# Kernel tuning notes

Measured on AMD Instinct MI355X. Metric: run time of the kernel, lower is better.

## Reference

```python
import jax, jax.numpy as jnp
import numpy as np

HEAD = 8
D_Q = 64
NEG_INF = -1e9
EPS = 1e-9


def setup_inputs() -> dict:
    key = jax.random.key(0)
    ks = jax.random.split(key, 5)
    bs, seq_len, d_model = 4, 1024, 512
    context = jax.random.normal(ks[0], (bs, seq_len, d_model), dtype=jnp.float32)
    attention_mask = jnp.ones((bs, seq_len), dtype=jnp.int32)
    # nn.Linear default init: U(-1/sqrt(fan_in), 1/sqrt(fan_in))
    bound = 1.0 / np.sqrt(d_model)
    Wq = jax.random.uniform(ks[1], (HEAD * D_Q, d_model), jnp.float32, -bound, bound)
    bq = jax.random.uniform(ks[2], (HEAD * D_Q,), jnp.float32, -bound, bound)
    Wk = jax.random.uniform(ks[3], (HEAD * D_Q, d_model), jnp.float32, -bound, bound)
    bk = jax.random.uniform(ks[4], (HEAD * D_Q,), jnp.float32, -bound, bound)
    return {"context": context, "attention_mask": attention_mask,
            "Wq": Wq, "bq": bq, "Wk": Wk, "bk": bk}


def reference(context, attention_mask, Wq, bq, Wk, bk):
    bs, seq_len, d_model = context.shape
    # structural masks
    after_mask = jnp.eye(seq_len, k=1, dtype=jnp.int32)    # superdiagonal
    prev_mask = jnp.eye(seq_len, k=-1, dtype=jnp.int32)    # subdiagonal
    self_mask = jnp.eye(seq_len, dtype=jnp.int32)          # diagonal
    summing_op = jnp.triu(jnp.ones((seq_len, seq_len), jnp.float32))  # upper-tri ones

    # attention_mask & (after + prev): (bs,1,1,S) & (S,S) -> (bs,1,S,S)
    mask = attention_mask[:, None, None, :] & (after_mask + prev_mask)

    # projections -> (bs, head, seq, d_q)
    q = (context @ Wq.T + bq).reshape(bs, seq_len, HEAD, D_Q).transpose(0, 2, 1, 3)
    k = (context @ Wk.T + bk).reshape(bs, seq_len, HEAD, D_Q).transpose(0, 2, 1, 3)

    scores = jnp.einsum('bhqd,bhkd->bhqk', q, k) / d_model
    scores = jnp.where(mask == 0, NEG_INF, scores)
    scores = jax.nn.softmax(scores, axis=-1)

    # geometric-mean fusion of forward/backward neighbor scores
    phrasal_attn = jnp.sqrt(scores * jnp.swapaxes(scores, -2, -1) + EPS)
    # prior_attn = 0 (default): phrasal_attn = 0 + (1-0)*phrasal_attn

    # log-cumsum via triangular matmuls
    p = jnp.where(after_mask == 0, 0.0, jnp.log(phrasal_attn + EPS))  # (bs,h,S,S)
    p = jnp.einsum('bhij,jk->bhik', p, summing_op)
    attn = jnp.exp(jnp.einsum('ij,bhjk->bhik', summing_op, p))
    # zero out on-and-below diagonal (keep strict upper triangle)
    strict_upper = summing_op.astype(jnp.int32) - self_mask
    attn = jnp.where(strict_upper == 0, 0.0, attn)
    attn = attn + jnp.swapaxes(attn, -2, -1) + jnp.where(self_mask == 0, EPS, phrasal_attn)
    return (attn, phrasal_attn)
```

## Files before the change

kernel.cpp:

```cpp
#include <hip/hip_runtime.h>
#include <hip/hip_bf16.h>

#define BS 4
#define SEQ 1024
#define DM 512
#define NQK 1024
#define NROW (BS*SEQ)
#define EPS 1e-9f
#define SQRTEPS 3.16227766e-5f

typedef __attribute__((ext_vector_type(8))) short short8;
typedef __attribute__((ext_vector_type(4))) float floatx4;

__global__ __launch_bounds__(256) void convert_kernel(
    const float* __restrict__ ctx, const float* __restrict__ Wq,
    const float* __restrict__ Wk, unsigned short* __restrict__ Xbf,
    unsigned short* __restrict__ Wbf)
{
    int idx = blockIdx.x * 256 + threadIdx.x;
    {
        unsigned int u = __float_as_uint(ctx[idx]);
        Xbf[idx] = (unsigned short)((u + 0x7fffu + ((u >> 16) & 1u)) >> 16);
    }
    if (idx < DM * DM) {
        unsigned int a = __float_as_uint(Wq[idx]);
        Wbf[idx] = (unsigned short)((a + 0x7fffu + ((a >> 16) & 1u)) >> 16);
        unsigned int c = __float_as_uint(Wk[idx]);
        Wbf[DM * DM + idx] = (unsigned short)((c + 0x7fffu + ((c >> 16) & 1u)) >> 16);
    }
}

#define BM 64
#define BN 64
#define BK 32
#define LDA 40

__global__ __launch_bounds__(256) void gemm_qk(
    const unsigned short* __restrict__ X, const unsigned short* __restrict__ W,
    const float* __restrict__ bq, const float* __restrict__ bk,
    float* __restrict__ QK)
{
    __shared__ unsigned short As[BM * LDA];
    __shared__ unsigned short Bs[BN * LDA];

    const int tid  = threadIdx.x;
    const int bm   = blockIdx.x;
    const int bn   = blockIdx.y;
    const int wave = tid >> 6;
    const int lane = tid & 63;
    const int wm   = wave >> 1, wn = wave & 1;
    const int lr   = lane & 15;
    const int kg   = lane >> 4;

    const int srow = tid >> 2;
    const int skc  = (tid & 3) << 3;
    const unsigned short* Xp = X + (size_t)(bm * BM + srow) * DM + skc;
    const unsigned short* Wp = W + (size_t)(bn * BN + srow) * DM + skc;

    floatx4 acc[2][2] = {};

    for (int k0 = 0; k0 < DM; k0 += BK) {
        uint4 va = *(const uint4*)(Xp + k0);
        uint4 vb = *(const uint4*)(Wp + k0);
        __syncthreads();
        *(uint4*)(As + srow * LDA + skc) = va;
        *(uint4*)(Bs + srow * LDA + skc) = vb;
        __syncthreads();

        short8 a[2], b[2];
        #pragma unroll
        for (int mi = 0; mi < 2; ++mi)
            a[mi] = *(const short8*)(As + (wm * 32 + mi * 16 + lr) * LDA + kg * 8);
        #pragma unroll
        for (int ni = 0; ni < 2; ++ni)
            b[ni] = *(const short8*)(Bs + (wn * 32 + ni * 16 + lr) * LDA + kg * 8);
        #pragma unroll
        for (int mi = 0; mi < 2; ++mi)
            #pragma unroll
            for (int ni = 0; ni < 2; ++ni)
                acc[mi][ni] = __builtin_amdgcn_mfma_f32_16x16x32_bf16(
                    a[mi], b[ni], acc[mi][ni], 0, 0, 0);
    }

    #pragma unroll
    for (int mi = 0; mi < 2; ++mi) {
        #pragma unroll
        for (int ni = 0; ni < 2; ++ni) {
            int n = bn * BN + wn * 32 + ni * 16 + lr;
            float bias = (n < DM) ? bq[n] : bk[n - DM];
            #pragma unroll
            for (int r = 0; r < 4; ++r) {
                int m = bm * BM + wm * 32 + mi * 16 + kg * 4 + r;
                QK[(size_t)m * NQK + n] = acc[mi][ni][r] + bias;
            }
        }
    }
}

__global__ __launch_bounds__(256) void dot_kernel(
    const float* __restrict__ QK, float* __restrict__ uArr, float* __restrict__ vArr)
{
    const int gw   = blockIdx.x * 4 + (threadIdx.x >> 6);
    const int lane = threadIdx.x & 63;
    const int bh   = gw >> 10;
    const int i    = gw & 1023;
    const int b    = bh >> 3, h = bh & 7;

    float u = 0.f, v = 0.f;
    if (i < SEQ - 1) {
        const float* r0 = QK + (size_t)(b * SEQ + i)     * NQK;
        const float* r1 = QK + (size_t)(b * SEQ + i + 1) * NQK;
        float qi  = r0[h * 64 + lane];
        float ki  = r0[DM + h * 64 + lane];
        float qi1 = r1[h * 64 + lane];
        float ki1 = r1[DM + h * 64 + lane];
        float pu = qi * ki1, pv = qi1 * ki;
        #pragma unroll
        for (int m = 1; m < 64; m <<= 1) {
            pu += __shfl_xor(pu, m);
            pv += __shfl_xor(pv, m);
        }
        u = pu * (1.0f / DM);
        v = pv * (1.0f / DM);
    }
    if (lane == 0) { uArr[gw] = u; vArr[gw] = v; }
}

__global__ __launch_bounds__(1024) void gscan_kernel(
    const float* __restrict__ uArr, const float* __restrict__ vArr,
    const int* __restrict__ am, float* __restrict__ gArr, float* __restrict__ CArr)
{
    __shared__ double wsum[16];

    const int bh   = blockIdx.x;
    const int b    = bh >> 3;
    const int i    = threadIdx.x;
    const int base = bh * SEQ;

    float g = 0.f;
    if (i < SEQ - 1) {
        float u   = uArr[base + i];
        float vv  = vArr[base + i];
        int   im1 = (i > 0) ? i - 1 : 0;
        float vm1 = vArr[base + im1];
        float up1 = uArr[base + i + 1];
        int mL = (i > 0) ? am[b * SEQ + i - 1] : 0;
        int mR = am[b * SEQ + i + 1];
        float s_up = mR ? (mL ? 1.f / (1.f + expf(vm1 - u)) : 1.f) : 0.f;
        int mL2 = am[b * SEQ + i];
        int mR2 = (i + 2 < SEQ) ? am[b * SEQ + i + 2] : 0;
        float s_dn = mL2 ? (mR2 ? 1.f / (1.f + expf(up1 - vv)) : 1.f) : 0.f;
        g = sqrtf(s_up * s_dn + EPS);
        gArr[base + i] = g;
    }

    double L = (i < SEQ - 1) ? (double)logf(g + EPS) : 0.0;
    double x = L;
    const int lane = i & 63, wv = i >> 6;
    #pragma unroll
    for (int off = 1; off < 64; off <<= 1) {
        double t = __shfl_up(x, off);
        if (lane >= off) x += t;
    }
    if (lane == 63) wsum[wv] = x;
    __syncthreads();
    double pref = 0.0;
    for (int w = 0; w < wv; ++w) pref += wsum[w];
    CArr[base + i] = (float)(pref + x - L);
}

__global__ __launch_bounds__(256) void fill_kernel(
    const float* __restrict__ gArr, const float* __restrict__ CArr,
    float* __restrict__ attn, float* __restrict__ phrasal)
{
    const int row = blockIdx.x;
    const int bh  = row >> 10;
    const int i   = row & 1023;
    const int t   = threadIdx.x;

    const float Ci  = CArr[row];
    const float gm1 = (i > 0)       ? gArr[bh * SEQ + i - 1] : 0.f;
    const float gp  = (i < SEQ - 1) ? gArr[bh * SEQ + i]     : 0.f;

    floatx4 c4 = *(const floatx4*)(CArr + bh * SEQ + t * 4);
    floatx4 av, pv;
    #pragma unroll
    for (int j = 0; j < 4; ++j) {
        int k = t * 4 + j;
        float ck = c4[j];
        float d  = (k > i) ? (ck - Ci) : (Ci - ck);
        av[j] = (k == i) ? SQRTEPS : (__expf(d) + EPS);
        pv[j] = (k == i - 1) ? gm1 : ((k == i + 1) ? gp : SQRTEPS);
    }
    *(floatx4*)(attn    + (size_t)row * SEQ + t * 4) = av;
    *(floatx4*)(phrasal + (size_t)row * SEQ + t * 4) = pv;
}

extern "C" void kernel_launch(void* const* d_in, const int* in_sizes, int n_in,
                              void* d_out, int out_size, void* d_ws, size_t ws_size,
                              hipStream_t stream) {
    const float* ctx = (const float*)d_in[0];
    const int*   am  = (const int*)d_in[1];
    const float* Wq  = (const float*)d_in[2];
    const float* bq  = (const float*)d_in[3];
    const float* Wk  = (const float*)d_in[4];
    const float* bk  = (const float*)d_in[5];
    float* out = (float*)d_out;

    char* ws = (char*)d_ws;
    unsigned short* Xbf = (unsigned short*)(ws);
    unsigned short* Wbf = (unsigned short*)(ws + 4194304);
    float*          QK  = (float*)(ws + 5242880);
    float*          uA  = (float*)(ws + 22020096);
    float*          vA  = (float*)(ws + 22151168);
    float*          gA  = (float*)(ws + 22282240);
    float*          CA  = (float*)(ws + 22413312);

    convert_kernel<<<dim3(BS * SEQ * DM / 256), 256, 0, stream>>>(ctx, Wq, Wk, Xbf, Wbf);
    gemm_qk<<<dim3(NROW / BM, NQK / BN), 256, 0, stream>>>(Xbf, Wbf, bq, bk, QK);
    dot_kernel<<<dim3(BS * 8 * SEQ / 4), 256, 0, stream>>>(QK, uA, vA);
    gscan_kernel<<<dim3(BS * 8), 1024, 0, stream>>>(uA, vA, am, gA, CA);

    float* attn_out    = out;
    float* phrasal_out = out + (size_t)BS * 8 * SEQ * SEQ;
    fill_kernel<<<dim3(BS * 8 * SEQ), 256, 0, stream>>>(gA, CA, attn_out, phrasal_out);
}
```

Baseline: 300.9 us.

## Overlap constant phrasal fill with GEMM blocks and patch diagonals later

Writing the constant background of the phrasal output moves out of the final fill kernel and into extra blocks appended to the QK GEMM launch, so that store traffic can run alongside the compute-bound GEMM. The fill kernel now writes only the attn matrix, and one thread per row patches the two off-diagonal phrasal entries afterwards. The fill kernel's write traffic is halved, but correctness now relies on launch ordering on the stream so the patches land after the background fill.

```diff
diff --git a/kernel.cpp b/kernel.cpp
--- a/kernel.cpp
+++ b/kernel.cpp
@@ -34,18 +34,32 @@
 #define BN 64
 #define BK 32
 #define LDA 40
-
-__global__ __launch_bounds__(256) void gemm_qk(
+#define NGEMM 1024
+#define NBG   4096
+
+__global__ __launch_bounds__(256) void gemm_qk_bg(
     const unsigned short* __restrict__ X, const unsigned short* __restrict__ W,
     const float* __restrict__ bq, const float* __restrict__ bk,
-    float* __restrict__ QK)
+    float* __restrict__ QK, float* __restrict__ phrasal)
 {
     __shared__ unsigned short As[BM * LDA];
     __shared__ unsigned short Bs[BN * LDA];
 
-    const int tid  = threadIdx.x;
-    const int bm   = blockIdx.x;
-    const int bn   = blockIdx.y;
+    const int id  = blockIdx.x;
+    const int tid = threadIdx.x;
+
+    if (id >= NGEMM) {
+        const int bb = id - NGEMM;
+        float* base = phrasal + (size_t)bb * 8192;
+        floatx4 v4 = {SQRTEPS, SQRTEPS, SQRTEPS, SQRTEPS};
+        #pragma unroll
+        for (int j = 0; j < 8; ++j)
+            *(floatx4*)(base + (size_t)(j * 256 + tid) * 4) = v4;
+        return;
+    }
+
+    const int bm   = id & 63;
+    const int bn   = id >> 6;
     const int wave = tid >> 6;
     const int lane = tid & 63;
     const int wm   = wave >> 1, wn = wave & 1;
@@ -169,7 +183,7 @@
     CArr[base + i] = (float)(pref + x - L);
 }
 
-__global__ __launch_bounds__(256) void fill_kernel(
+__global__ __launch_bounds__(256) void fill_attn(
     const float* __restrict__ gArr, const float* __restrict__ CArr,
     float* __restrict__ attn, float* __restrict__ phrasal)
 {
@@ -178,22 +192,23 @@
     const int i   = row & 1023;
     const int t   = threadIdx.x;
 
-    const float Ci  = CArr[row];
-    const float gm1 = (i > 0)       ? gArr[bh * SEQ + i - 1] : 0.f;
-    const float gp  = (i < SEQ - 1) ? gArr[bh * SEQ + i]     : 0.f;
-
+    const float Ci = CArr[row];
     floatx4 c4 = *(const floatx4*)(CArr + bh * SEQ + t * 4);
-    floatx4 av, pv;
+    floatx4 av;
     #pragma unroll
     for (int j = 0; j < 4; ++j) {
         int k = t * 4 + j;
-        float ck = c4[j];
-        float d  = (k > i) ? (ck - Ci) : (Ci - ck);
+        float d = (k > i) ? (c4[j] - Ci) : (Ci - c4[j]);
         av[j] = (k == i) ? SQRTEPS : (__expf(d) + EPS);
-        pv[j] = (k == i - 1) ? gm1 : ((k == i + 1) ? gp : SQRTEPS);
-    }
-    *(floatx4*)(attn    + (size_t)row * SEQ + t * 4) = av;
-    *(floatx4*)(phrasal + (size_t)row * SEQ + t * 4) = pv;
+    }
+    *(floatx4*)(attn + (size_t)row * SEQ + t * 4) = av;
+
+    if (t == 0) {
+        if (i > 0)
+            phrasal[(size_t)row * SEQ + i - 1] = gArr[bh * SEQ + i - 1];
+        if (i < SEQ - 1)
+            phrasal[(size_t)row * SEQ + i + 1] = gArr[bh * SEQ + i];
+    }
 }
 
 extern "C" void kernel_launch(void* const* d_in, const int* in_sizes, int n_in,
@@ -216,12 +231,12 @@
     float*          gA  = (float*)(ws + 22282240);
     float*          CA  = (float*)(ws + 22413312);
 
+    float* attn_out    = out;
+    float* phrasal_out = out + (size_t)BS * 8 * SEQ * SEQ;
+
     convert_kernel<<<dim3(BS * SEQ * DM / 256), 256, 0, stream>>>(ctx, Wq, Wk, Xbf, Wbf);
-    gemm_qk<<<dim3(NROW / BM, NQK / BN), 256, 0, stream>>>(Xbf, Wbf, bq, bk, QK);
+    gemm_qk_bg<<<dim3(NGEMM + NBG), 256, 0, stream>>>(Xbf, Wbf, bq, bk, QK, phrasal_out);
     dot_kernel<<<dim3(BS * 8 * SEQ / 4), 256, 0, stream>>>(QK, uA, vA);
     gscan_kernel<<<dim3(BS * 8), 1024, 0, stream>>>(uA, vA, am, gA, CA);
-
-    float* attn_out    = out;
-    float* phrasal_out = out + (size_t)BS * 8 * SEQ * SEQ;
-    fill_kernel<<<dim3(BS * 8 * SEQ), 256, 0, stream>>>(gA, CA, attn_out, phrasal_out);
-}
+    fill_attn<<<dim3(BS * 8 * SEQ), 256, 0, stream>>>(gA, CA, attn_out, phrasal_out);
+}
```

New measurement: 293.6 us. 1.02x faster.
